# Kernel optimization log

Measured on AMD Instinct MI355X. Metric: run time of the kernel, lower is better.

Reference implementation:

```python
import jax, jax.numpy as jnp
import numpy as np

K = 3  # kernel_size; stride=1, padding=1 so num_D=D, num_H=H, num_W=W


def _neighborhood_diff(x):
    """For each voxel, (center - each of its 27 zero-padded 3x3x3 neighbors).

    Equivalent to F.interpolate(x, scale_factor=3, 'nearest') - overlap_expand3D(x)
    reshaped to [B, C, D, 3, H, 3, W, 3]: out[..., d, kd, h, kh, w, kw] =
    x[d,h,w] - x_pad[d+kd, h+kh, w+kw].
    """
    B, C, D, H, W = x.shape
    xp = jnp.pad(x, ((0, 0), (0, 0), (1, 1), (1, 1), (1, 1)))
    # gather shifted copies along each spatial dim (27 static slices)
    p = jnp.stack([xp[:, :, kd:kd + D] for kd in range(K)], axis=3)            # B,C,D,3,H+2,W+2
    p = jnp.stack([p[:, :, :, :, kh:kh + H] for kh in range(K)], axis=5)       # B,C,D,3,H,3,W+2
    p = jnp.stack([p[..., kw:kw + W] for kw in range(K)], axis=7)              # B,C,D,3,H,3,W,3
    center = x[:, :, :, None, :, None, :, None]                                # nearest-upsample, factored
    return center - p


def setup_inputs() -> dict:
    key = jax.random.key(0)
    k1, k2 = jax.random.split(key)
    shape = (2, 1, 32, 128, 128)  # B, C, D, H, W
    x = jax.random.normal(k1, shape, dtype=jnp.float32)
    y = jax.random.normal(k2, shape, dtype=jnp.float32)
    return {"x": x, "y": y}


def reference(x, y):
    x_diff = _neighborhood_diff(x)
    y_diff = _neighborhood_diff(y)
    return jnp.mean(jnp.abs(x_diff - y_diff))
```

## Files before the change

### kernel.cpp

```cpp
#include <hip/hip_runtime.h>

constexpr int Dd = 32, Hh = 128, Ww = 128, Bv = 2;
constexpr int NVOX = Bv * Dd * Hh * Ww;
constexpr int BLK  = 512;
constexpr int BLKF = 256;

constexpr int TD = 2, TH = 4;
constexpr int ZT = Dd / TD;
constexpr int YT = Hh / TH;
constexpr int NBLK = Bv * ZT * YT;
constexpr int LSTR = 136;
constexpr int RZ = TD + 2, RY = TH + 2;
constexpr int NROWS = RZ * RY;
constexpr int NF2   = LSTR / 2;
constexpr int NITEM = NROWS * NF2;

__global__ void __launch_bounds__(BLK, 8)
cdl_worker(const float* __restrict__ xg, const float* __restrict__ yg,
           float* __restrict__ partials)
{
    __shared__ float lds[NROWS * LSTR];
    __shared__ float smem[BLK / 64];

    const int tid = threadIdx.x;
    const int bid = (blockIdx.x & 7) * (NBLK / 8) + (blockIdx.x >> 3);

    int t = bid;
    const int yt  = t & (YT - 1); t >>= 5;
    const int zt  = t & (ZT - 1); t >>= 4;
    const int vol = t;
    const int z0 = zt * TD, y0 = yt * TH;
    const size_t vbase = (size_t)vol * Dd * Hh * Ww;

#pragma unroll
    for (int p = 0; p < 4; ++p) {
        const int idx = p * BLK + tid;
        if (idx < NITEM) {
            const int row  = idx / NF2;
            const int slot = idx - row * NF2;
            const int lzr  = row / RY;
            const int lyr  = row - lzr * RY;
            const int gz = z0 + lzr - 1;
            const int gy = y0 + lyr - 1;
            const int w  = 2 * slot - 4;
            float2 v = make_float2(0.f, 0.f);
            if ((unsigned)gz < (unsigned)Dd && (unsigned)gy < (unsigned)Hh &&
                (unsigned)w <= 126u) {
                const size_t g = vbase + ((size_t)gz * Hh + gy) * Ww + w;
                const float2 a = *(const float2*)(xg + g);
                const float2 b = *(const float2*)(yg + g);
                v = make_float2(a.x - b.x, a.y - b.y);
            }
            *(float2*)&lds[row * LSTR + 2 * slot] = v;
        }
    }
    __syncthreads();

    const int j  = tid & 63;
    const int r  = tid >> 6;
    const int lz = r >> 2;
    const int ly = r & 3;
    const int k0 = 2 * j + 4;

    const float2 c = *(const float2*)&lds[((lz + 1) * RY + (ly + 1)) * LSTR + k0];

    float s = 0.f;
#pragma unroll
    for (int dz = 0; dz < 3; ++dz) {
#pragma unroll
        for (int dy = 0; dy < 3; ++dy) {
            const float* rp = &lds[((lz + dz) * RY + (ly + dy)) * LSTR];
            const float2 M = *(const float2*)&rp[k0 - 2];
            const float2 A = *(const float2*)&rp[k0];
            const float2 Q = *(const float2*)&rp[k0 + 2];
            s += fabsf(c.x - M.y) + fabsf(c.x - A.x) + fabsf(c.x - A.y);
            s += fabsf(c.y - A.x) + fabsf(c.y - A.y) + fabsf(c.y - Q.x);
        }
    }

    const int lane = tid & 63;
    const int wid  = tid >> 6;
#pragma unroll
    for (int off = 32; off > 0; off >>= 1) s += __shfl_down(s, off, 64);
    if (lane == 0) smem[wid] = s;
    __syncthreads();
    if (tid == 0) {
        float tsum = 0.f;
#pragma unroll
        for (int w = 0; w < BLK / 64; ++w) tsum += smem[w];
        partials[bid] = tsum;
    }
}

__global__ void __launch_bounds__(BLKF)
cdl_finish(const float* __restrict__ partials, float* __restrict__ out)
{
    float acc = 0.f;
#pragma unroll
    for (int i = 0; i < NBLK / BLKF; ++i)
        acc += partials[i * BLKF + threadIdx.x];
#pragma unroll
    for (int off = 32; off > 0; off >>= 1) acc += __shfl_down(acc, off, 64);

    __shared__ float smem[BLKF / 64];
    const int lane = threadIdx.x & 63;
    const int wid  = threadIdx.x >> 6;
    if (lane == 0) smem[wid] = acc;
    __syncthreads();
    if (threadIdx.x == 0) {
        const double tot = (double)smem[0] + (double)smem[1] +
                           (double)smem[2] + (double)smem[3];
        out[0] = (float)(tot / (27.0 * (double)NVOX));
    }
}

extern "C" void kernel_launch(void* const* d_in, const int* in_sizes, int n_in,
                              void* d_out, int out_size, void* d_ws, size_t ws_size,
                              hipStream_t stream) {
    const float* x  = (const float*)d_in[0];
    const float* y  = (const float*)d_in[1];
    float* partials = (float*)d_ws;
    float* out      = (float*)d_out;

    cdl_worker<<<NBLK, BLK, 0, stream>>>(x, y, partials);
    cdl_finish<<<1, BLKF, 0, stream>>>(partials, out);
}
```

Before: 12.32 us.

## Exploit pair symmetry of neighbor differences to halve stencil work and halo

Uses the symmetry |d(p)-d(q)| = |d(q)-d(p)| to count each interior neighbor pair once (13 forward directions) and double the sum. A per-voxel correction term covers the asymmetric zero-padded boundary neighbors. The shared-memory tile drops one z halo plane (RZ from 4 to 3), which cuts global loads and LDS reads. The cost is extra boundary-flag arithmetic and a more delicate correctness argument at the volume edges.

Result: faster. 11.49 us, median of 2 (-6.8%).

```diff
diff --git a/kernel.cpp b/kernel.cpp
--- a/kernel.cpp
+++ b/kernel.cpp
@@ -10,10 +10,14 @@
 constexpr int YT = Hh / TH;
 constexpr int NBLK = Bv * ZT * YT;
 constexpr int LSTR = 136;
-constexpr int RZ = TD + 2, RY = TH + 2;
+constexpr int RZ = TD + 1, RY = TH + 2;
 constexpr int NROWS = RZ * RY;
 constexpr int NF2   = LSTR / 2;
 constexpr int NITEM = NROWS * NF2;
+
+__device__ __constant__ const signed char DIRZ[13] = {1,1,1, 1,1,1, 1,1,1, 0,0,0, 0};
+__device__ __constant__ const signed char DIRY[13] = {-1,-1,-1, 0,0,0, 1,1,1, 1,1,1, 0};
+__device__ __constant__ const signed char DIRW[13] = {-1,0,1, -1,0,1, -1,0,1, -1,0,1, 1};
 
 __global__ void __launch_bounds__(BLK, 8)
 cdl_worker(const float* __restrict__ xg, const float* __restrict__ yg,
@@ -33,14 +37,14 @@
     const size_t vbase = (size_t)vol * Dd * Hh * Ww;
 
 #pragma unroll
-    for (int p = 0; p < 4; ++p) {
+    for (int p = 0; p < 3; ++p) {
         const int idx = p * BLK + tid;
         if (idx < NITEM) {
             const int row  = idx / NF2;
             const int slot = idx - row * NF2;
             const int lzr  = row / RY;
             const int lyr  = row - lzr * RY;
-            const int gz = z0 + lzr - 1;
+            const int gz = z0 + lzr;
             const int gy = y0 + lyr - 1;
             const int w  = 2 * slot - 4;
             float2 v = make_float2(0.f, 0.f);
@@ -62,21 +66,48 @@
     const int ly = r & 3;
     const int k0 = 2 * j + 4;
 
-    const float2 c = *(const float2*)&lds[((lz + 1) * RY + (ly + 1)) * LSTR + k0];
+    const float2 c = *(const float2*)&lds[(lz * RY + ly + 1) * LSTR + k0];
 
-    float s = 0.f;
+    float sp = 0.f;
+    {
+        const float Qx = lds[(lz * RY + ly + 1) * LSTR + k0 + 2];
+        sp += fabsf(c.x - c.y) + fabsf(c.y - Qx);
+    }
+#define ROW6(RP) do { const float* rp_ = (RP);                              \
+        const float2 M = *(const float2*)&rp_[k0 - 2];                      \
+        const float2 A = *(const float2*)&rp_[k0];                          \
+        const float2 Q = *(const float2*)&rp_[k0 + 2];                      \
+        sp += fabsf(c.x - M.y) + fabsf(c.x - A.x) + fabsf(c.x - A.y);       \
+        sp += fabsf(c.y - A.x) + fabsf(c.y - A.y) + fabsf(c.y - Q.x);      \
+    } while (0)
+    ROW6(&lds[(lz * RY + ly + 2) * LSTR]);
+    ROW6(&lds[((lz + 1) * RY + ly    ) * LSTR]);
+    ROW6(&lds[((lz + 1) * RY + ly + 1) * LSTR]);
+    ROW6(&lds[((lz + 1) * RY + ly + 2) * LSTR]);
+#undef ROW6
+
+    const int gz = z0 + lz, gy = y0 + ly;
+    const bool zl = (gz == 0), zh = (gz == Dd - 1);
+    const bool yl = (gy == 0), yh = (gy == Hh - 1);
+    const bool wlx = (j == 0);
+    const bool why = (j == 63);
+    int ndx = 0, ndy = 0;
 #pragma unroll
-    for (int dz = 0; dz < 3; ++dz) {
-#pragma unroll
-        for (int dy = 0; dy < 3; ++dy) {
-            const float* rp = &lds[((lz + dz) * RY + (ly + dy)) * LSTR];
-            const float2 M = *(const float2*)&rp[k0 - 2];
-            const float2 A = *(const float2*)&rp[k0];
-            const float2 Q = *(const float2*)&rp[k0 + 2];
-            s += fabsf(c.x - M.y) + fabsf(c.x - A.x) + fabsf(c.x - A.y);
-            s += fabsf(c.y - A.x) + fabsf(c.y - A.y) + fabsf(c.y - Q.x);
-        }
+    for (int q = 0; q < 13; ++q) {
+        const int oz = DIRZ[q], oy = DIRY[q], ow = DIRW[q];
+        const bool bpx = (oz > 0 && zh) || (oy > 0 && yh) || (oy < 0 && yl)
+                       || (ow < 0 && wlx);
+        const bool bmx = (oz > 0 && zl) || (oy > 0 && yl) || (oy < 0 && yh)
+                       || (ow > 0 && wlx);
+        const bool bpy = (oz > 0 && zh) || (oy > 0 && yh) || (oy < 0 && yl)
+                       || (ow > 0 && why);
+        const bool bmy = (oz > 0 && zl) || (oy > 0 && yl) || (oy < 0 && yh)
+                       || (ow < 0 && why);
+        ndx += (int)bmx - (int)bpx;
+        ndy += (int)bmy - (int)bpy;
     }
+
+    float s = 2.f * sp + fabsf(c.x) * (float)ndx + fabsf(c.y) * (float)ndy;
 
     const int lane = tid & 63;
     const int wid  = tid >> 6;
```
